# Performance work log

Measured on AMD Instinct MI355X. Metric: run time of the kernel, lower is better.

## Reference

```python
import jax, jax.numpy as jnp
import numpy as np
import math

S, B, H, NH, HD = 2048, 1, 4096, 32, 128
ROT = HD // 2  # 2D RoPE: each half of head_dim gets its own rotary embedding


def _rotate_half(x):
    x1, x2 = jnp.split(x, 2, axis=-1)
    return jnp.concatenate((-x2, x1), axis=-1)


def _rope_tables(max_pos, dim):
    inv_freq = 1.0 / (10000.0 ** (jnp.arange(0, dim, 2, dtype=jnp.float32) / dim))
    freqs = jnp.arange(max_pos, dtype=jnp.float32)[:, None] * inv_freq[None, :]  # [P, dim/2]
    emb = jnp.concatenate((freqs, freqs), axis=-1)  # [P, dim]
    return jnp.cos(emb), jnp.sin(emb)


def _apply_rope(q, k, cos_t, sin_t, pid):
    # q,k: [S,B,NH,ROT]; pid: [S,B]
    c = cos_t[pid][:, :, None, :]  # [S,B,1,ROT]
    s = sin_t[pid][:, :, None, :]
    return q * c + _rotate_half(q) * s, k * c + _rotate_half(k) * s


def setup_inputs() -> dict:
    key = jax.random.key(0)
    k1, k2, k3, k4, k5 = jax.random.split(key, 5)
    hidden_states = jax.random.normal(k1, (S, B, H), dtype=jnp.float32)
    pos = jnp.arange(S, dtype=jnp.int32)[None, :]          # [1,S] standard positions
    blk = jnp.zeros((1, S), dtype=jnp.int32)                # block positions (pre-gmask all zeros)
    position_ids = jnp.stack([pos, blk], axis=1)            # [B,2,S]
    # causal mask: True = masked out
    attention_mask = jnp.triu(jnp.ones((S, S), dtype=bool), k=1)[None, None]  # [B,1,S,S]
    Wqkv = jax.random.normal(k2, (3 * H, H), dtype=jnp.float32) * 0.02
    bqkv = jax.random.normal(k3, (3 * H,), dtype=jnp.float32) * 0.02
    Wd = jax.random.normal(k4, (H, H), dtype=jnp.float32) * 0.02
    bd = jax.random.normal(k5, (H,), dtype=jnp.float32) * 0.02
    return {"hidden_states": hidden_states, "position_ids": position_ids,
            "attention_mask": attention_mask, "layer_id": 5,
            "Wqkv": Wqkv, "bqkv": bqkv, "Wd": Wd, "bd": bd}


def reference(hidden_states, position_ids, attention_mask, layer_id, Wqkv, bqkv, Wd, bd):
    # QKV projection: [S,B,H] -> [S,B,NH,3*HD]
    mixed = hidden_states @ Wqkv.T + bqkv
    mixed = mixed.reshape(S, B, NH, 3 * HD)
    q, k, v = jnp.split(mixed, 3, axis=-1)  # each [S,B,NH,HD]

    # 2D rotary position embedding on the two head-dim halves
    q1, q2 = jnp.split(q, 2, axis=-1)
    k1, k2 = jnp.split(k, 2, axis=-1)
    cos_t, sin_t = _rope_tables(S, ROT)
    pid = position_ids[:, 0, :].T   # [S,B]
    bid = position_ids[:, 1, :].T   # [S,B]
    q1, k1 = _apply_rope(q1, k1, cos_t, sin_t, pid)
    q2, k2 = _apply_rope(q2, k2, cos_t, sin_t, bid)
    q = jnp.concatenate([q1, q2], axis=-1)
    k = jnp.concatenate([k1, k2], axis=-1)

    # layer-scaled attention scores
    coeff = float(layer_id + 1)
    q = q / (math.sqrt(HD) * coeff)
    scores = jnp.einsum('sbnd,tbnd->bnst', q, k)  # [B,NH,S,S]
    scores = jnp.where(attention_mask, jnp.float32(-10000.0), scores)
    scores = scores.astype(jnp.float32) * coeff
    probs = jax.nn.softmax(scores, axis=-1).astype(hidden_states.dtype)

    ctx = jnp.einsum('bnst,tbnd->sbnd', probs, v).reshape(S, B, NH * HD)
    return ctx @ Wd.T + bd  # [S,B,H]
```

## Files before the change

### kernel.cpp

```cpp
#include <hip/hip_runtime.h>


#define S_LEN 2048
#define NHEAD 32
#define HDIM 128
#define HID 4096

typedef float f32x4 __attribute__((ext_vector_type(4)));
typedef __bf16 bf16x8 __attribute__((ext_vector_type(8)));
typedef __bf16 bf16x4 __attribute__((ext_vector_type(4)));
typedef _Float16 f16x4 __attribute__((ext_vector_type(4)));
typedef _Float16 f16x8 __attribute__((ext_vector_type(8)));

__device__ __forceinline__ void gload16(const void* g, void* l) {
  __builtin_amdgcn_global_load_lds(
      (const __attribute__((address_space(1))) void*)g,
      (__attribute__((address_space(3))) void*)l, 16, 0, 0);
}

__device__ __forceinline__ void cvt4(const float* in, __bf16* out, int i) {
  f32x4 v = *(const f32x4*)(in + (size_t)i * 4);
  bf16x4 o;
  o[0] = (__bf16)v[0]; o[1] = (__bf16)v[1];
  o[2] = (__bf16)v[2]; o[3] = (__bf16)v[3];
  *(bf16x4*)(out + (size_t)i * 4) = o;
}

__global__ __launch_bounds__(256) void cvt2_kernel(
    const float* __restrict__ in1, __bf16* __restrict__ out1, int n4_1,
    const float* __restrict__ in2, __bf16* __restrict__ out2, int n4_2) {
  int i = blockIdx.x * 256 + threadIdx.x;
  if (i < n4_1) {
    cvt4(in1, out1, i);
  } else if (i - n4_1 < n4_2) {
    cvt4(in2, out2, i - n4_1);
  }
}

template <int UNITS>
__device__ __forceinline__ void stage_rows(const __bf16* __restrict__ G,
                                           int grow0, int Kstride, int kofs,
                                           __bf16* lds, int tid) {
#pragma unroll
  for (int i = 0; i < UNITS; ++i) {
    int idx = i * 512 + tid;
    int rr = idx >> 3;
    int offp = (idx & 7) * 16;
    int off = offp ^ ((rr & 7) << 4);
    const char* src =
        (const char*)(G + (size_t)(grow0 + rr) * Kstride + kofs) + off;
    char* dst = (char*)lds + idx * 16;
    gload16(src, dst);
  }
}

__device__ __forceinline__ bf16x8 ldsfrag(const __bf16* hb, int rowin, int ks,
                                          int lg) {
  int off = ((ks * 64 + lg * 16) ^ ((rowin & 7) << 4));
  return *(const bf16x8*)((const char*)hb + rowin * 128 + off);
}

#define READ_A(DST, SLOT)                                                     \
  _Pragma("unroll") for (int mi = 0; mi < 4; ++mi)                            \
      _Pragma("unroll") for (int ks = 0; ks < 2; ++ks) DST[mi][ks] =          \
      ldsfrag(SLOT, wm * 64 + mi * 16 + lr, ks, lg);

#define READ_B(DST, SLOT)                                                     \
  _Pragma("unroll") for (int nj = 0; nj < 2; ++nj)                            \
      _Pragma("unroll") for (int ks = 0; ks < 2; ++ks) DST[nj][ks] =          \
      ldsfrag(SLOT, wn * 32 + nj * 16 + lr, ks, lg);

#define MFMA_Q(MH, NH, AFR, BFR)                                              \
  __builtin_amdgcn_s_setprio(1);                                              \
  _Pragma("unroll") for (int mi = 0; mi < 4; ++mi)                            \
      _Pragma("unroll") for (int nj = 0; nj < 2; ++nj)                        \
          _Pragma("unroll") for (int ks = 0; ks < 2; ++ks)                    \
              acc[MH][NH][mi][nj] =                                           \
      __builtin_amdgcn_mfma_f32_16x16x32_bf16(AFR[mi][ks], BFR[nj][ks],       \
                                              acc[MH][NH][mi][nj], 0, 0, 0);  \
  __builtin_amdgcn_s_setprio(0);

#define BAR asm volatile("s_barrier" ::: "memory");

__global__ __launch_bounds__(512, 2) void gemm256_kernel(
    const __bf16* __restrict__ A, const __bf16* __restrict__ B,
    const float* __restrict__ bias, __bf16* __restrict__ Cout, int M, int N,
    int K, int mtiles) {
  __shared__ __align__(16) __bf16 As[2][2][128 * 64];
  __shared__ __align__(16) __bf16 Bs[2][2][128 * 64];
  const int tid = threadIdx.x;
  int bid = blockIdx.x;
  int per_patch = mtiles * 8;
  int p = bid / per_patch, r = bid % per_patch;
  int mt = r % mtiles, nt = p * 8 + r / mtiles;
  int m0 = mt * 256, n0 = nt * 256;
  const int wid = tid >> 6, l = tid & 63;
  const int wm = wid >> 2, wn = wid & 3;
  const int lr = l & 15, lg = l >> 4;
  const int nk = K >> 6;

  f32x4 acc[2][2][4][2];
#pragma unroll
  for (int a = 0; a < 2; ++a)
#pragma unroll
    for (int b = 0; b < 2; ++b)
#pragma unroll
      for (int c = 0; c < 4; ++c)
#pragma unroll
        for (int d = 0; d < 2; ++d) acc[a][b][c][d] = 0.f;

  stage_rows<2>(A, m0, K, 0, &As[0][0][0], tid);
  stage_rows<2>(B, n0, K, 0, &Bs[0][0][0], tid);
  stage_rows<2>(B, n0 + 128, K, 0, &Bs[0][1][0], tid);
  stage_rows<2>(A, m0 + 128, K, 0, &As[0][1][0], tid);
  if (nk > 1) {
    stage_rows<2>(A, m0, K, 64, &As[1][0][0], tid);
    stage_rows<2>(B, n0, K, 64, &Bs[1][0][0], tid);
    stage_rows<2>(B, n0 + 128, K, 64, &Bs[1][1][0], tid);
    asm volatile("s_waitcnt vmcnt(6)" ::: "memory");
  } else {
    asm volatile("s_waitcnt vmcnt(0)" ::: "memory");
  }
  BAR;

  for (int t = 0; t < nk; ++t) {
    const int cur = t & 1, nxt = cur ^ 1;
    const int kt1 = (t + 1) * 64;
    const int kt2 = (t + 2) * 64;
    const bool s1 = (t + 1 < nk), s2 = (t + 2 < nk);
    bf16x8 a[4][2], b0[2][2], b1[2][2];

    READ_A(a, &As[cur][0][0]);
    READ_B(b0, &Bs[cur][0][0]);
    if (s1) stage_rows<2>(A, m0 + 128, K, kt1, &As[nxt][1][0], tid);
    BAR;
    MFMA_Q(0, 0, a, b0);

    READ_B(b1, &Bs[cur][1][0]);
    if (s2) stage_rows<2>(A, m0, K, kt2, &As[cur][0][0], tid);
    BAR;
    MFMA_Q(0, 1, a, b1);

    READ_A(a, &As[cur][1][0]);
    if (s2) stage_rows<2>(B, n0 + 128, K, kt2, &Bs[cur][1][0], tid);
    BAR;
    MFMA_Q(1, 1, a, b1);

    if (s2) stage_rows<2>(B, n0, K, kt2, &Bs[cur][0][0], tid);
    BAR;
    MFMA_Q(1, 0, a, b0);
    if (s2)
      asm volatile("s_waitcnt vmcnt(6)" ::: "memory");
    else
      asm volatile("s_waitcnt vmcnt(0)" ::: "memory");
  }

#pragma unroll
  for (int mh = 0; mh < 2; ++mh)
#pragma unroll
    for (int nh = 0; nh < 2; ++nh)
#pragma unroll
      for (int mi = 0; mi < 4; ++mi)
#pragma unroll
        for (int nj = 0; nj < 2; ++nj) {
          int row = m0 + mh * 128 + wm * 64 + mi * 16 + lg * 4;
          int col = n0 + nh * 128 + wn * 32 + nj * 16 + lr;
          float bv = bias[col];
          f32x4 v = acc[mh][nh][mi][nj];
#pragma unroll
          for (int j = 0; j < 4; ++j)
            Cout[(size_t)(row + j) * N + col] = (__bf16)(v[j] + bv);
        }
}

__global__ __launch_bounds__(512, 2) void gemm128_kernel(
    const __bf16* __restrict__ A, const __bf16* __restrict__ B,
    const float* __restrict__ bias, float* __restrict__ Cout, int M, int N,
    int K, int mtiles) {
  __shared__ __align__(16) __bf16 As[2][128 * 64];
  __shared__ __align__(16) __bf16 Bs[2][2][128 * 64];
  const int tid = threadIdx.x;
  int bid = blockIdx.x;
  int per_patch = mtiles * 8;
  int p = bid / per_patch, r = bid % per_patch;
  int mt = r % mtiles, nt = p * 8 + r / mtiles;
  int m0 = mt * 128, n0 = nt * 256;
  const int wid = tid >> 6, l = tid & 63;
  const int wm = wid >> 2, wn = wid & 3;
  const int lr = l & 15, lg = l >> 4;
  const int nk = K >> 6;

  f32x4 acc[4][4];
#pragma unroll
  for (int a = 0; a < 4; ++a)
#pragma unroll
    for (int b = 0; b < 4; ++b) acc[a][b] = 0.f;

  const int bhalf = wn >> 1;
  const int br0 = (wn & 1) * 64;

  stage_rows<2>(A, m0, K, 0, &As[0][0], tid);
  stage_rows<2>(B, n0, K, 0, &Bs[0][0][0], tid);
  stage_rows<2>(B, n0 + 128, K, 0, &Bs[0][1][0], tid);
  stage_rows<2>(A, m0, K, 64, &As[1][0], tid);
  stage_rows<2>(B, n0, K, 64, &Bs[1][0][0], tid);
  stage_rows<2>(B, n0 + 128, K, 64, &Bs[1][1][0], tid);
  asm volatile("s_waitcnt vmcnt(6)" ::: "memory");
  BAR;

  for (int t = 0; t < nk; ++t) {
    const int cur = t & 1;
    const int kt2 = (t + 2) * 64;
    const bool s2 = (t + 2 < nk);
    const __bf16* bslot = &Bs[cur][bhalf][0];
    bf16x8 a0[4], b0[4], a1[4], b1[4];

#pragma unroll
    for (int mi = 0; mi < 4; ++mi)
      a0[mi] = ldsfrag(&As[cur][0], wm * 64 + mi * 16 + lr, 0, lg);
#pragma unroll
    for (int nj = 0; nj < 4; ++nj)
      b0[nj] = ldsfrag(bslot, br0 + nj * 16 + lr, 0, lg);
    BAR;
    __builtin_amdgcn_s_setprio(1);
#pragma unroll
    for (int mi = 0; mi < 4; ++mi)
#pragma unroll
      for (int nj = 0; nj < 4; ++nj)
        acc[mi][nj] = __builtin_amdgcn_mfma_f32_16x16x32_bf16(
            a0[mi], b0[nj], acc[mi][nj], 0, 0, 0);
    __builtin_amdgcn_s_setprio(0);

#pragma unroll
    for (int mi = 0; mi < 4; ++mi)
      a1[mi] = ldsfrag(&As[cur][0], wm * 64 + mi * 16 + lr, 1, lg);
#pragma unroll
    for (int nj = 0; nj < 4; ++nj)
      b1[nj] = ldsfrag(bslot, br0 + nj * 16 + lr, 1, lg);
    BAR;
    if (s2) {
      stage_rows<2>(A, m0, K, kt2, &As[cur][0], tid);
      stage_rows<2>(B, n0, K, kt2, &Bs[cur][0][0], tid);
      stage_rows<2>(B, n0 + 128, K, kt2, &Bs[cur][1][0], tid);
    }
    __builtin_amdgcn_s_setprio(1);
#pragma unroll
    for (int mi = 0; mi < 4; ++mi)
#pragma unroll
      for (int nj = 0; nj < 4; ++nj)
        acc[mi][nj] = __builtin_amdgcn_mfma_f32_16x16x32_bf16(
            a1[mi], b1[nj], acc[mi][nj], 0, 0, 0);
    __builtin_amdgcn_s_setprio(0);
    if (s2)
      asm volatile("s_waitcnt vmcnt(6)" ::: "memory");
    else
      asm volatile("s_waitcnt vmcnt(0)" ::: "memory");
  }

#pragma unroll
  for (int mi = 0; mi < 4; ++mi)
#pragma unroll
    for (int nj = 0; nj < 4; ++nj) {
      int row = m0 + wm * 64 + mi * 16 + lg * 4;
      int col = n0 + wn * 64 + nj * 16 + lr;
      float bv = bias[col];
      f32x4 v = acc[mi][nj];
#pragma unroll
      for (int j = 0; j < 4; ++j)
        Cout[(size_t)(row + j) * N + col] = v[j] + bv;
    }
}

__global__ __launch_bounds__(256) void rope_kernel(
    const __bf16* __restrict__ qkv, const int* __restrict__ pos_ids,
    __bf16* __restrict__ Q, __bf16* __restrict__ K, _Float16* __restrict__ VT) {
  int h = blockIdx.x & 31, sb = blockIdx.x >> 5;
  int s0 = sb * 64;
  int t = threadIdx.x;
  __shared__ float cs[64][2][2][32];
  __shared__ _Float16 vs[64][132];

  for (int idx = t; idx < 64 * 64; idx += 256) {
    int sl = idx >> 6, half = (idx >> 5) & 1, i = idx & 31;
    int p = pos_ids[half * S_LEN + s0 + sl];
    float f = powf(10000.f, -(float)i / 32.f);
    float ang = (float)p * f;
    cs[sl][half][0][i] = cosf(ang);
    cs[sl][half][1][i] = sinf(ang);
  }
#pragma unroll
  for (int c = 0; c < 4; c++) {
    int chunk = c * 256 + t;
    int slv = chunk >> 4, co = (chunk & 15) * 8;
    const __bf16* vsrc =
        qkv + (size_t)(s0 + slv) * (NHEAD * 3 * HDIM) + h * 384 + 256 + co;
    bf16x8 vv = *(const bf16x8*)vsrc;
    f16x4 a, b;
#pragma unroll
    for (int j = 0; j < 4; j++) {
      a[j] = (_Float16)(float)vv[j];
      b[j] = (_Float16)(float)vv[4 + j];
    }
    *(f16x4*)&vs[slv][co] = a;
    *(f16x4*)&vs[slv][co + 4] = b;
  }
  __syncthreads();

  {
    int sl = t >> 2, role = t & 3;
    int isK = role >> 1, half = role & 1;
    const __bf16* src = qkv + (size_t)(s0 + sl) * (NHEAD * 3 * HDIM) + h * 384 +
                        isK * 128 + half * 64;
    float scale = isK ? 1.f : 0.08838834764831845f;
    float x[64];
    bf16x8 buf[8];
#pragma unroll
    for (int c = 0; c < 8; c++) buf[c] = *(const bf16x8*)(src + c * 8);
#pragma unroll
    for (int c = 0; c < 8; c++)
#pragma unroll
      for (int j = 0; j < 8; j++) x[c * 8 + j] = (float)buf[c][j];
    bf16x8 ob[8];
#pragma unroll
    for (int i = 0; i < 64; i++) {
      int ii = i & 31;
      float cv = cs[sl][half][0][ii], sv = cs[sl][half][1][ii];
      float partner = (i < 32) ? x[i + 32] : x[i - 32];
      float sgn = (i < 32) ? -1.f : 1.f;
      float o = (x[i] * cv + sgn * partner * sv) * scale;
      ob[i >> 3][i & 7] = (__bf16)o;
    }
    __bf16* dst = (isK ? K : Q) + ((size_t)h * S_LEN + s0 + sl) * HDIM + half * 64;
#pragma unroll
    for (int c = 0; c < 8; c++) *(bf16x8*)(dst + c * 8) = ob[c];
  }

#pragma unroll
  for (int c = 0; c < 4; c++) {
    int chunk = c * 256 + t;
    int d = chunk >> 3, so = (chunk & 7) * 8;
    f16x8 o;
#pragma unroll
    for (int j = 0; j < 8; j++) o[j] = vs[so + j][d];
    *(f16x8*)(VT + ((size_t)h * HDIM + d) * S_LEN + s0 + so) = o;
  }
}

__global__ __launch_bounds__(256, 2) void attn_kernel(
    const __bf16* __restrict__ Q, const __bf16* __restrict__ K,
    const _Float16* __restrict__ VT, __bf16* __restrict__ ctx,
    const float* __restrict__ Wd, __bf16* __restrict__ wdb) {
  int b = blockIdx.x;
  if (b >= 512) {
    const int n4 = HID * HID / 4;
    for (int i = (b - 512) * 256 + threadIdx.x; i < n4; i += 128 * 256)
      cvt4(Wd, wdb, i);
    return;
  }
  int h = b & 31;
  int x = b >> 5;
  int qb = (b < 256) ? (15 - x) : (x - 8);
  int w = threadIdx.x >> 6, l = threadIdx.x & 63;
  int lr = l & 15, lg = l >> 4;
  int q0 = qb * 128 + w * 32;
  const __bf16* Qh = Q + (size_t)h * S_LEN * HDIM;
  const __bf16* Kh = K + (size_t)h * S_LEN * HDIM;
  const _Float16* Vh = VT + (size_t)h * HDIM * S_LEN;

  bf16x8 qfA[4], qfB[4];
#pragma unroll
  for (int kk = 0; kk < 4; kk++) {
    qfA[kk] = *(const bf16x8*)(Qh + (size_t)(q0 + lr) * HDIM + kk * 32 + lg * 8);
    qfB[kk] =
        *(const bf16x8*)(Qh + (size_t)(q0 + 16 + lr) * HDIM + kk * 32 + lg * 8);
  }

  f32x4 accA[8], accB[8];
#pragma unroll
  for (int tt = 0; tt < 8; tt++) { accA[tt] = 0.f; accB[tt] = 0.f; }
  float mA = -INFINITY, lsA = 0.f, mB = -INFINITY, lsB = 0.f;
  int qgA = q0 + lr, qgB = q0 + 16 + lr;
  int qmax = q0 + 31;

  for (int kv0 = 0; kv0 <= qmax; kv0 += 32) {
    f32x4 stA0 = 0.f, stA1 = 0.f, stB0 = 0.f, stB1 = 0.f;
#pragma unroll
    for (int kk = 0; kk < 4; kk++) {
      bf16x8 kf0 =
          *(const bf16x8*)(Kh + (size_t)(kv0 + lr) * HDIM + kk * 32 + lg * 8);
      bf16x8 kf1 = *(const bf16x8*)(Kh + (size_t)(kv0 + 16 + lr) * HDIM +
                                    kk * 32 + lg * 8);
      stA0 = __builtin_amdgcn_mfma_f32_16x16x32_bf16(kf0, qfA[kk], stA0, 0, 0, 0);
      stB0 = __builtin_amdgcn_mfma_f32_16x16x32_bf16(kf0, qfB[kk], stB0, 0, 0, 0);
      stA1 = __builtin_amdgcn_mfma_f32_16x16x32_bf16(kf1, qfA[kk], stA1, 0, 0, 0);
      stB1 = __builtin_amdgcn_mfma_f32_16x16x32_bf16(kf1, qfB[kk], stB1, 0, 0, 0);
    }

    f16x4 vb0[8], vb1[8];
#pragma unroll
    for (int tt = 0; tt < 8; tt++) {
      const _Float16* vcol = Vh + (size_t)(tt * 16 + lr) * S_LEN;
      vb0[tt] = *(const f16x4*)(vcol + kv0 + lg * 4);
      vb1[tt] = *(const f16x4*)(vcol + kv0 + 16 + lg * 4);
    }

    float tmA = -INFINITY, tmB = -INFINITY;
#pragma unroll
    for (int j = 0; j < 4; j++) {
      int kvg0 = kv0 + lg * 4 + j;
      int kvg1 = kvg0 + 16;
      if (kvg0 > qgA) stA0[j] = -INFINITY;
      if (kvg1 > qgA) stA1[j] = -INFINITY;
      if (kvg0 > qgB) stB0[j] = -INFINITY;
      if (kvg1 > qgB) stB1[j] = -INFINITY;
      tmA = fmaxf(tmA, fmaxf(stA0[j], stA1[j]));
      tmB = fmaxf(tmB, fmaxf(stB0[j], stB1[j]));
    }
    tmA = fmaxf(tmA, __shfl_xor(tmA, 16));
    tmA = fmaxf(tmA, __shfl_xor(tmA, 32));
    tmB = fmaxf(tmB, __shfl_xor(tmB, 16));
    tmB = fmaxf(tmB, __shfl_xor(tmB, 32));
    int need = __any((tmA > mA) || (tmB > mB));
    float mnA = fmaxf(mA, tmA), mnB = fmaxf(mB, tmB);

    f16x4 paA0, paA1, paB0, paB1;
    float tsA = 0.f, tsB = 0.f;
#pragma unroll
    for (int j = 0; j < 4; j++) {
      float pA0 = __expf(stA0[j] - mnA);
      float pA1 = __expf(stA1[j] - mnA);
      float pB0 = __expf(stB0[j] - mnB);
      float pB1 = __expf(stB1[j] - mnB);
      tsA += pA0 + pA1;
      tsB += pB0 + pB1;
      paA0[j] = (_Float16)pA0; paA1[j] = (_Float16)pA1;
      paB0[j] = (_Float16)pB0; paB1[j] = (_Float16)pB1;
    }
    tsA += __shfl_xor(tsA, 16);
    tsA += __shfl_xor(tsA, 32);
    tsB += __shfl_xor(tsB, 16);
    tsB += __shfl_xor(tsB, 32);

    if (need) {
      float scA = __expf(mA - mnA), scB = __expf(mB - mnB);
      lsA = lsA * scA + tsA;
      lsB = lsB * scB + tsB;
      float sAj[4], sBj[4];
#pragma unroll
      for (int j = 0; j < 4; j++) {
        sAj[j] = __shfl(scA, lg * 4 + j);
        sBj[j] = __shfl(scB, lg * 4 + j);
      }
#pragma unroll
      for (int tt = 0; tt < 8; tt++)
#pragma unroll
        for (int j = 0; j < 4; j++) {
          accA[tt][j] *= sAj[j];
          accB[tt][j] *= sBj[j];
        }
    } else {
      lsA += tsA;
      lsB += tsB;
    }
    mA = mnA; mB = mnB;

#pragma unroll
    for (int tt = 0; tt < 8; tt++) {
      accA[tt] =
          __builtin_amdgcn_mfma_f32_16x16x16f16(paA0, vb0[tt], accA[tt], 0, 0, 0);
      accB[tt] =
          __builtin_amdgcn_mfma_f32_16x16x16f16(paB0, vb0[tt], accB[tt], 0, 0, 0);
      accA[tt] =
          __builtin_amdgcn_mfma_f32_16x16x16f16(paA1, vb1[tt], accA[tt], 0, 0, 0);
      accB[tt] =
          __builtin_amdgcn_mfma_f32_16x16x16f16(paB1, vb1[tt], accB[tt], 0, 0, 0);
    }
  }

  float rA[4], rB[4];
#pragma unroll
  for (int j = 0; j < 4; j++) {
    rA[j] = 1.f / __shfl(lsA, lg * 4 + j);
    rB[j] = 1.f / __shfl(lsB, lg * 4 + j);
  }
#pragma unroll
  for (int tt = 0; tt < 8; tt++) {
#pragma unroll
    for (int j = 0; j < 4; j++) {
      int qoA = q0 + lg * 4 + j;
      int qoB = q0 + 16 + lg * 4 + j;
      ctx[(size_t)qoA * (NHEAD * HDIM) + h * HDIM + tt * 16 + lr] =
          (__bf16)(accA[tt][j] * rA[j]);
      ctx[(size_t)qoB * (NHEAD * HDIM) + h * HDIM + tt * 16 + lr] =
          (__bf16)(accB[tt][j] * rB[j]);
    }
  }
}

extern "C" void kernel_launch(void* const* d_in, const int* in_sizes, int n_in,
                              void* d_out, int out_size, void* d_ws,
                              size_t ws_size, hipStream_t stream) {
  const float* hs = (const float*)d_in[0];
  const int* pos_ids = (const int*)d_in[1];
  const float* Wqkv = (const float*)d_in[4];
  const float* bqkv = (const float*)d_in[5];
  const float* Wd = (const float*)d_in[6];
  const float* bd = (const float*)d_in[7];
  float* out = (float*)d_out;

  char* ws = (char*)d_ws;
  constexpr size_t OFF_W = 16777216ULL;
  constexpr size_t OFF_QKV = OFF_W + 100663296ULL;
  constexpr size_t OFF_Q = OFF_QKV + 50331648ULL;
  constexpr size_t OFF_K = OFF_Q + 16777216ULL;
  constexpr size_t OFF_V = OFF_K + 16777216ULL;
  __bf16* hsb = (__bf16*)(ws);
  __bf16* wqkvb = (__bf16*)(ws + OFF_W);
  __bf16* wdb = (__bf16*)(ws + OFF_W);
  __bf16* qkvb = (__bf16*)(ws + OFF_QKV);
  __bf16* ctxb = qkvb;
  __bf16* Qb = (__bf16*)(ws + OFF_Q);
  __bf16* Kb = (__bf16*)(ws + OFF_K);
  _Float16* Vtb = (_Float16*)(ws + OFF_V);

  const int n4_hs = S_LEN * HID / 4;
  const int n4_w = 3 * HID * HID / 4;
  cvt2_kernel<<<(n4_hs + n4_w + 255) / 256, 256, 0, stream>>>(
      hs, hsb, n4_hs, Wqkv, wqkvb, n4_w);

  gemm256_kernel<<<8 * 48, 512, 0, stream>>>(hsb, wqkvb, bqkv, qkvb, S_LEN,
                                             3 * HID, HID, 8);

  rope_kernel<<<NHEAD * (S_LEN / 64), 256, 0, stream>>>(qkvb, pos_ids, Qb, Kb,
                                                        Vtb);

  attn_kernel<<<512 + 128, 256, 0, stream>>>(Qb, Kb, Vtb, ctxb, Wd, wdb);

  gemm128_kernel<<<16 * 16, 512, 0, stream>>>(ctxb, wdb, bd, out, S_LEN, HID,
                                              HID, 16);
}
```

Before: 576.1 us.

## Halve per-wave query rows in attention to double blocks and occupancy

Each wave of the attention kernel now handles 16 query rows instead of 32, so the grid grows to 1024 attention blocks with a four-group ordering that pairs long and short causal rows. Launch bounds rise to 4 blocks per CU, and V fragments are loaded inside the PV MFMA loop rather than prefetched into registers. This cuts register pressure and raises occupancy and parallelism. The cost is that each K/V tile loaded from global memory is reused by half as many query rows, roughly doubling K/V traffic, and V loads are now less overlapped with the softmax math.

New measurement: 755.5 us. +31.1%, slower.

```diff
diff --git a/kernel.cpp b/kernel.cpp
--- a/kernel.cpp
+++ b/kernel.cpp
@@ -346,153 +346,114 @@
   }
 }
 
-__global__ __launch_bounds__(256, 2) void attn_kernel(
+__global__ __launch_bounds__(256, 4) void attn_kernel(
     const __bf16* __restrict__ Q, const __bf16* __restrict__ K,
     const _Float16* __restrict__ VT, __bf16* __restrict__ ctx,
     const float* __restrict__ Wd, __bf16* __restrict__ wdb) {
   int b = blockIdx.x;
-  if (b >= 512) {
+  if (b >= 1024) {
     const int n4 = HID * HID / 4;
-    for (int i = (b - 512) * 256 + threadIdx.x; i < n4; i += 128 * 256)
+    for (int i = (b - 1024) * 256 + threadIdx.x; i < n4; i += 128 * 256)
       cvt4(Wd, wdb, i);
     return;
   }
   int h = b & 31;
   int x = b >> 5;
-  int qb = (b < 256) ? (15 - x) : (x - 8);
+  int xi = x & 7, g = x >> 3;
+  int qb = (g == 0) ? 31 - xi : (g == 1) ? xi : (g == 2) ? 23 - xi : 8 + xi;
   int w = threadIdx.x >> 6, l = threadIdx.x & 63;
   int lr = l & 15, lg = l >> 4;
-  int q0 = qb * 128 + w * 32;
+  int q0 = qb * 64 + w * 16;
   const __bf16* Qh = Q + (size_t)h * S_LEN * HDIM;
   const __bf16* Kh = K + (size_t)h * S_LEN * HDIM;
   const _Float16* Vh = VT + (size_t)h * HDIM * S_LEN;
 
-  bf16x8 qfA[4], qfB[4];
-#pragma unroll
-  for (int kk = 0; kk < 4; kk++) {
-    qfA[kk] = *(const bf16x8*)(Qh + (size_t)(q0 + lr) * HDIM + kk * 32 + lg * 8);
-    qfB[kk] =
-        *(const bf16x8*)(Qh + (size_t)(q0 + 16 + lr) * HDIM + kk * 32 + lg * 8);
-  }
-
-  f32x4 accA[8], accB[8];
-#pragma unroll
-  for (int tt = 0; tt < 8; tt++) { accA[tt] = 0.f; accB[tt] = 0.f; }
-  float mA = -INFINITY, lsA = 0.f, mB = -INFINITY, lsB = 0.f;
-  int qgA = q0 + lr, qgB = q0 + 16 + lr;
-  int qmax = q0 + 31;
+  bf16x8 qf[4];
+#pragma unroll
+  for (int kk = 0; kk < 4; kk++)
+    qf[kk] = *(const bf16x8*)(Qh + (size_t)(q0 + lr) * HDIM + kk * 32 + lg * 8);
+
+  f32x4 acc[8];
+#pragma unroll
+  for (int tt = 0; tt < 8; tt++) acc[tt] = 0.f;
+  float m = -INFINITY, ls = 0.f;
+  int qg = q0 + lr;
+  int qmax = q0 + 15;
 
   for (int kv0 = 0; kv0 <= qmax; kv0 += 32) {
-    f32x4 stA0 = 0.f, stA1 = 0.f, stB0 = 0.f, stB1 = 0.f;
+    f32x4 st0 = 0.f, st1 = 0.f;
 #pragma unroll
     for (int kk = 0; kk < 4; kk++) {
       bf16x8 kf0 =
           *(const bf16x8*)(Kh + (size_t)(kv0 + lr) * HDIM + kk * 32 + lg * 8);
       bf16x8 kf1 = *(const bf16x8*)(Kh + (size_t)(kv0 + 16 + lr) * HDIM +
                                     kk * 32 + lg * 8);
-      stA0 = __builtin_amdgcn_mfma_f32_16x16x32_bf16(kf0, qfA[kk], stA0, 0, 0, 0);
-      stB0 = __builtin_amdgcn_mfma_f32_16x16x32_bf16(kf0, qfB[kk], stB0, 0, 0, 0);
-      stA1 = __builtin_amdgcn_mfma_f32_16x16x32_bf16(kf1, qfA[kk], stA1, 0, 0, 0);
-      stB1 = __builtin_amdgcn_mfma_f32_16x16x32_bf16(kf1, qfB[kk], stB1, 0, 0, 0);
-    }
-
-    f16x4 vb0[8], vb1[8];
-#pragma unroll
-    for (int tt = 0; tt < 8; tt++) {
-      const _Float16* vcol = Vh + (size_t)(tt * 16 + lr) * S_LEN;
-      vb0[tt] = *(const f16x4*)(vcol + kv0 + lg * 4);
-      vb1[tt] = *(const f16x4*)(vcol + kv0 + 16 + lg * 4);
-    }
-
-    float tmA = -INFINITY, tmB = -INFINITY;
+      st0 = __builtin_amdgcn_mfma_f32_16x16x32_bf16(kf0, qf[kk], st0, 0, 0, 0);
+      st1 = __builtin_amdgcn_mfma_f32_16x16x32_bf16(kf1, qf[kk], st1, 0, 0, 0);
+    }
+
+    float tm = -INFINITY;
 #pragma unroll
     for (int j = 0; j < 4; j++) {
       int kvg0 = kv0 + lg * 4 + j;
       int kvg1 = kvg0 + 16;
-      if (kvg0 > qgA) stA0[j] = -INFINITY;
-      if (kvg1 > qgA) stA1[j] = -INFINITY;
-      if (kvg0 > qgB) stB0[j] = -INFINITY;
-      if (kvg1 > qgB) stB1[j] = -INFINITY;
-      tmA = fmaxf(tmA, fmaxf(stA0[j], stA1[j]));
-      tmB = fmaxf(tmB, fmaxf(stB0[j], stB1[j]));
-    }
-    tmA = fmaxf(tmA, __shfl_xor(tmA, 16));
-    tmA = fmaxf(tmA, __shfl_xor(tmA, 32));
-    tmB = fmaxf(tmB, __shfl_xor(tmB, 16));
-    tmB = fmaxf(tmB, __shfl_xor(tmB, 32));
-    int need = __any((tmA > mA) || (tmB > mB));
-    float mnA = fmaxf(mA, tmA), mnB = fmaxf(mB, tmB);
-
-    f16x4 paA0, paA1, paB0, paB1;
-    float tsA = 0.f, tsB = 0.f;
+      if (kvg0 > qg) st0[j] = -INFINITY;
+      if (kvg1 > qg) st1[j] = -INFINITY;
+      tm = fmaxf(tm, fmaxf(st0[j], st1[j]));
+    }
+    tm = fmaxf(tm, __shfl_xor(tm, 16));
+    tm = fmaxf(tm, __shfl_xor(tm, 32));
+    int need = __any(tm > m);
+    float mn = fmaxf(m, tm);
+
+    f16x4 pa0, pa1;
+    float ts = 0.f;
 #pragma unroll
     for (int j = 0; j < 4; j++) {
-      float pA0 = __expf(stA0[j] - mnA);
-      float pA1 = __expf(stA1[j] - mnA);
-      float pB0 = __expf(stB0[j] - mnB);
-      float pB1 = __expf(stB1[j] - mnB);
-      tsA += pA0 + pA1;
-      tsB += pB0 + pB1;
-      paA0[j] = (_Float16)pA0; paA1[j] = (_Float16)pA1;
-      paB0[j] = (_Float16)pB0; paB1[j] = (_Float16)pB1;
-    }
-    tsA += __shfl_xor(tsA, 16);
-    tsA += __shfl_xor(tsA, 32);
-    tsB += __shfl_xor(tsB, 16);
-    tsB += __shfl_xor(tsB, 32);
+      float p0 = __expf(st0[j] - mn);
+      float p1 = __expf(st1[j] - mn);
+      ts += p0 + p1;
+      pa0[j] = (_Float16)p0;
+      pa1[j] = (_Float16)p1;
+    }
+    ts += __shfl_xor(ts, 16);
+    ts += __shfl_xor(ts, 32);
 
     if (need) {
-      float scA = __expf(mA - mnA), scB = __expf(mB - mnB);
-      lsA = lsA * scA + tsA;
-      lsB = lsB * scB + tsB;
-      float sAj[4], sBj[4];
-#pragma unroll
-      for (int j = 0; j < 4; j++) {
-        sAj[j] = __shfl(scA, lg * 4 + j);
-        sBj[j] = __shfl(scB, lg * 4 + j);
-      }
+      float sc = __expf(m - mn);
+      ls = ls * sc + ts;
+      float sj[4];
+#pragma unroll
+      for (int j = 0; j < 4; j++) sj[j] = __shfl(sc, lg * 4 + j);
 #pragma unroll
       for (int tt = 0; tt < 8; tt++)
 #pragma unroll
-        for (int j = 0; j < 4; j++) {
-          accA[tt][j] *= sAj[j];
-          accB[tt][j] *= sBj[j];
-        }
+        for (int j = 0; j < 4; j++) acc[tt][j] *= sj[j];
     } else {
-      lsA += tsA;
-      lsB += tsB;
-    }
-    mA = mnA; mB = mnB;
+      ls += ts;
+    }
+    m = mn;
 
 #pragma unroll
     for (int tt = 0; tt < 8; tt++) {
-      accA[tt] =
-          __builtin_amdgcn_mfma_f32_16x16x16f16(paA0, vb0[tt], accA[tt], 0, 0, 0);
-      accB[tt] =
-          __builtin_amdgcn_mfma_f32_16x16x16f16(paB0, vb0[tt], accB[tt], 0, 0, 0);
-      accA[tt] =
-          __builtin_amdgcn_mfma_f32_16x16x16f16(paA1, vb1[tt], accA[tt], 0, 0, 0);
-      accB[tt] =
-          __builtin_amdgcn_mfma_f32_16x16x16f16(paB1, vb1[tt], accB[tt], 0, 0, 0);
-    }
-  }
-
-  float rA[4], rB[4];
-#pragma unroll
-  for (int j = 0; j < 4; j++) {
-    rA[j] = 1.f / __shfl(lsA, lg * 4 + j);
-    rB[j] = 1.f / __shfl(lsB, lg * 4 + j);
-  }
+      const _Float16* vcol = Vh + (size_t)(tt * 16 + lr) * S_LEN;
+      f16x4 vb0 = *(const f16x4*)(vcol + kv0 + lg * 4);
+      f16x4 vb1 = *(const f16x4*)(vcol + kv0 + 16 + lg * 4);
+      acc[tt] = __builtin_amdgcn_mfma_f32_16x16x16f16(pa0, vb0, acc[tt], 0, 0, 0);
+      acc[tt] = __builtin_amdgcn_mfma_f32_16x16x16f16(pa1, vb1, acc[tt], 0, 0, 0);
+    }
+  }
+
+  float rj[4];
+#pragma unroll
+  for (int j = 0; j < 4; j++) rj[j] = 1.f / __shfl(ls, lg * 4 + j);
 #pragma unroll
   for (int tt = 0; tt < 8; tt++) {
 #pragma unroll
     for (int j = 0; j < 4; j++) {
-      int qoA = q0 + lg * 4 + j;
-      int qoB = q0 + 16 + lg * 4 + j;
-      ctx[(size_t)qoA * (NHEAD * HDIM) + h * HDIM + tt * 16 + lr] =
-          (__bf16)(accA[tt][j] * rA[j]);
-      ctx[(size_t)qoB * (NHEAD * HDIM) + h * HDIM + tt * 16 + lr] =
-          (__bf16)(accB[tt][j] * rB[j]);
+      int qo = q0 + lg * 4 + j;
+      ctx[(size_t)qo * (NHEAD * HDIM) + h * HDIM + tt * 16 + lr] =
+          (__bf16)(acc[tt][j] * rj[j]);
     }
   }
 }
@@ -534,7 +495,7 @@
   rope_kernel<<<NHEAD * (S_LEN / 64), 256, 0, stream>>>(qkvb, pos_ids, Qb, Kb,
                                                         Vtb);
 
-  attn_kernel<<<512 + 128, 256, 0, stream>>>(Qb, Kb, Vtb, ctxb, Wd, wdb);
+  attn_kernel<<<1024 + 128, 256, 0, stream>>>(Qb, Kb, Vtb, ctxb, Wd, wdb);
 
   gemm128_kernel<<<16 * 16, 512, 0, stream>>>(ctxb, wdb, bd, out, S_LEN, HID,
                                               HID, 16);
```
